# Kernel optimization log

Measured on AMD Instinct MI355X. Metric: run time of the kernel, lower is better.

Reference implementation:

```python
import jax, jax.numpy as jnp
import numpy as np

V, S, B, D, H, DH, FF = 98304, 1536, 2, 768, 24, 32, 3072
SCALE = 1.0 / float(np.sqrt(DH))  # 0.17677669529663687


def _ln(x, w, b, eps=1e-5):
    mu = jnp.mean(x, axis=-1, keepdims=True)
    var = jnp.mean(jnp.square(x - mu), axis=-1, keepdims=True)
    return (x - mu) * jax.lax.rsqrt(var + eps) * w + b


def _block(x, mask, ln1w, ln1b, wqkv, bqkv, wo, bo, ln2w, ln2b, wfc, bfc, wproj, bproj):
    # x: (S, B, D) Megatron layout; mask: (B, 1, S, S) bool, True = masked
    h = _ln(x, ln1w, ln1b)
    qkv = (h @ wqkv.T + bqkv).reshape(S, B, H, 3 * DH)  # interleaved q/k/v per head
    q, k, v = qkv[..., :DH], qkv[..., DH:2 * DH], qkv[..., 2 * DH:]
    q = jnp.transpose(q, (1, 2, 0, 3))  # (B, H, S, DH)
    k = jnp.transpose(k, (1, 2, 0, 3))
    v = jnp.transpose(v, (1, 2, 0, 3))
    scores = jnp.einsum('bhqd,bhkd->bhqk', q, k) * SCALE  # (B, H, S, S)
    scores = jnp.where(mask, jnp.float32(-10000.0), scores)
    p = jax.nn.softmax(scores, axis=-1)
    ctx = jnp.einsum('bhqk,bhkd->bhqd', p, v)
    ctx = jnp.transpose(ctx, (2, 0, 1, 3)).reshape(S, B, D)  # back to (S, B, D)
    x = x + ctx @ wo.T + bo  # attention residual (dropout treated as identity)
    h2 = _ln(x, ln2w, ln2b)
    m = jax.nn.gelu(h2 @ wfc.T + bfc, approximate=False)  # exact (erf) gelu as aten.gelu
    return x + m @ wproj.T + bproj


def _param_shapes():
    ps = [('wte', (V, D)), ('wpe', (S, D))]
    for l in ('l0', 'l1'):
        ps += [(l + '_ln1_w', (D,)), (l + '_ln1_b', (D,)),
               (l + '_wqkv', (3 * D, D)), (l + '_bqkv', (3 * D,)),
               (l + '_wo', (D, D)), (l + '_bo', (D,)),
               (l + '_ln2_w', (D,)), (l + '_ln2_b', (D,)),
               (l + '_wfc', (FF, D)), (l + '_bfc', (FF,)),
               (l + '_wproj', (D, FF)), (l + '_bproj', (D,))]
    ps += [('lnf_w', (D,)), ('lnf_b', (D,))]
    return ps


def setup_inputs() -> dict:
    key = jax.random.key(0)
    inp = {}
    inp['input_ids'] = jax.random.randint(jax.random.fold_in(key, 0), (B, S), 0, V, dtype=jnp.int32)
    inp['position_ids'] = jnp.broadcast_to(jnp.arange(S, dtype=jnp.int32), (B, S))
    causal = jnp.triu(jnp.ones((S, S), jnp.bool_), k=1)  # True above diagonal = masked
    inp['attn_mask'] = jnp.broadcast_to(causal, (B, 1, S, S))
    for i, (name, shape) in enumerate(_param_shapes()):
        k = jax.random.fold_in(key, 100 + i)
        if name in ('lnf_w',) or (('_ln' in name) and name.endswith('_w')):
            inp[name] = jnp.ones(shape, jnp.float32)
        else:
            inp[name] = jax.random.normal(k, shape, jnp.float32) * 0.02
    return inp


def reference(input_ids, position_ids, attn_mask,
              wte, wpe,
              l0_ln1_w, l0_ln1_b, l0_wqkv, l0_bqkv, l0_wo, l0_bo,
              l0_ln2_w, l0_ln2_b, l0_wfc, l0_bfc, l0_wproj, l0_bproj,
              l1_ln1_w, l1_ln1_b, l1_wqkv, l1_bqkv, l1_wo, l1_bo,
              l1_ln2_w, l1_ln2_b, l1_wfc, l1_bfc, l1_wproj, l1_bproj,
              lnf_w, lnf_b):
    x = wte[input_ids] + wpe[position_ids]  # (B, S, D)
    x = jnp.transpose(x, (1, 0, 2))  # (S, B, D)
    x = _block(x, attn_mask, l0_ln1_w, l0_ln1_b, l0_wqkv, l0_bqkv, l0_wo, l0_bo,
               l0_ln2_w, l0_ln2_b, l0_wfc, l0_bfc, l0_wproj, l0_bproj)
    x = _block(x, attn_mask, l1_ln1_w, l1_ln1_b, l1_wqkv, l1_bqkv, l1_wo, l1_bo,
               l1_ln2_w, l1_ln2_b, l1_wfc, l1_bfc, l1_wproj, l1_bproj)
    return _ln(x, lnf_w, lnf_b)  # (S, B, D)
```

## Files before the change

### kernel.cpp

```cpp
#include <hip/hip_runtime.h>
#include <cmath>
#include <type_traits>

typedef unsigned short u16;
typedef float  f32x4 __attribute__((ext_vector_type(4)));
typedef short  s16x8 __attribute__((ext_vector_type(8)));
typedef __bf16 b16x8 __attribute__((ext_vector_type(8)));

#define GLOBAL_AS __attribute__((address_space(1)))
#define LDS_AS    __attribute__((address_space(3)))

constexpr int S_  = 1536;
constexpr int B_  = 2;
constexpr int D_  = 768;
constexpr int H_  = 24;
constexpr int DH_ = 32;
constexpr int FF_ = 3072;
constexpr int N_  = S_ * B_;
constexpr int D3_ = 3 * D_;
constexpr float SCALE_ = 0.17677669529663687f;

template <typename T>
static __device__ inline auto mfma_try(T a, T b, f32x4 c, int)
    -> decltype(__builtin_amdgcn_mfma_f32_16x16x32_bf16(a, b, c, 0, 0, 0)) {
  return __builtin_amdgcn_mfma_f32_16x16x32_bf16(a, b, c, 0, 0, 0);
}
template <typename T>
static __device__ inline f32x4 mfma_try(T a, T b, f32x4 c, long) {
  b16x8 ab = __builtin_bit_cast(b16x8, a);
  b16x8 bb = __builtin_bit_cast(b16x8, b);
  return __builtin_amdgcn_mfma_f32_16x16x32_bf16(ab, bb, c, 0, 0, 0);
}
static __device__ inline f32x4 mfma_bf16(s16x8 a, s16x8 b, f32x4 c) {
  return mfma_try(a, b, c, 0);
}

static __device__ inline u16 f2bf(float f) {
  unsigned u = __builtin_bit_cast(unsigned, f);
  return (u16)((u + 0x7FFFu + ((u >> 16) & 1u)) >> 16);
}

static __device__ inline float rmax16(float v) {
  v = fmaxf(v, __shfl_xor(v, 1));
  v = fmaxf(v, __shfl_xor(v, 2));
  v = fmaxf(v, __shfl_xor(v, 4));
  v = fmaxf(v, __shfl_xor(v, 8));
  return v;
}
static __device__ inline float rsum16(float v) {
  v += __shfl_xor(v, 1);
  v += __shfl_xor(v, 2);
  v += __shfl_xor(v, 4);
  v += __shfl_xor(v, 8);
  return v;
}

__global__ void convert_weights_kernel(const float* __restrict__ wqkv,
                                       const float* __restrict__ wo,
                                       const float* __restrict__ wfc,
                                       const float* __restrict__ wproj,
                                       u16* __restrict__ dst) {
  constexpr int C0 = D3_ * D_;
  constexpr int C1 = C0 + D_ * D_;
  constexpr int C2 = C1 + FF_ * D_;
  constexpr int C3 = C2 + D_ * FF_;
  int i4 = (blockIdx.x * 256 + threadIdx.x) * 4;
  if (i4 >= C3) return;
  const float* src; int off;
  if (i4 < C0)      { src = wqkv;  off = i4; }
  else if (i4 < C1) { src = wo;    off = i4 - C0; }
  else if (i4 < C2) { src = wfc;   off = i4 - C1; }
  else              { src = wproj; off = i4 - C2; }
  float4 v = *(const float4*)(src + off);
  ushort4 o;
  o.x = f2bf(v.x); o.y = f2bf(v.y); o.z = f2bf(v.z); o.w = f2bf(v.w);
  *(ushort4*)(dst + i4) = o;
}

__global__ void embed_kernel(const int* __restrict__ ids, const int* __restrict__ pos,
                             const float* __restrict__ wte, const float* __restrict__ wpe,
                             float* __restrict__ x) {
  int g  = blockIdx.x * 256 + threadIdx.x;
  int i4 = g * 4;
  int row = i4 / D_;
  int d   = i4 - row * D_;
  int s = row >> 1, b = row & 1;
  int t = ids[b * S_ + s];
  int p = pos[b * S_ + s];
  float4 a = *(const float4*)(wte + (size_t)t * D_ + d);
  float4 c = *(const float4*)(wpe + (size_t)p * D_ + d);
  a.x += c.x; a.y += c.y; a.z += c.z; a.w += c.w;
  *(float4*)(x + i4) = a;
}

template <typename OUT>
__global__ void ln_kernel(const float* __restrict__ x, const float* __restrict__ w,
                          const float* __restrict__ b, OUT* __restrict__ out) {
  int wid = threadIdx.x >> 6, lane = threadIdx.x & 63;
  int tok = blockIdx.x * 4 + wid;
  const float* xr = x + (size_t)tok * D_;
  float4 v[3];
  float s = 0.f, ss = 0.f;
#pragma unroll
  for (int c = 0; c < 3; ++c) {
    v[c] = *(const float4*)(xr + c * 256 + lane * 4);
    s  += v[c].x + v[c].y + v[c].z + v[c].w;
    ss += v[c].x * v[c].x + v[c].y * v[c].y + v[c].z * v[c].z + v[c].w * v[c].w;
  }
#pragma unroll
  for (int m = 1; m <= 32; m <<= 1) { s += __shfl_xor(s, m); ss += __shfl_xor(ss, m); }
  float mu = s * (1.0f / D_);
  float var = ss * (1.0f / D_) - mu * mu;
  float rs = rsqrtf(var + 1e-5f);
#pragma unroll
  for (int c = 0; c < 3; ++c) {
    int d = c * 256 + lane * 4;
    float o0 = (v[c].x - mu) * rs * w[d + 0] + b[d + 0];
    float o1 = (v[c].y - mu) * rs * w[d + 1] + b[d + 1];
    float o2 = (v[c].z - mu) * rs * w[d + 2] + b[d + 2];
    float o3 = (v[c].w - mu) * rs * w[d + 3] + b[d + 3];
    if constexpr (std::is_same_v<OUT, u16>) {
      ushort4 o; o.x = f2bf(o0); o.y = f2bf(o1); o.z = f2bf(o2); o.w = f2bf(o3);
      *(ushort4*)(out + (size_t)tok * D_ + d) = o;
    } else {
      float4 o; o.x = o0; o.y = o1; o.z = o2; o.w = o3;
      *(float4*)(out + (size_t)tok * D_ + d) = o;
    }
  }
}

template <int BM, int BN, int EPI>
__launch_bounds__(256, 3)
__global__ void gemm_kernel(const u16* __restrict__ X, const u16* __restrict__ W,
                            const float* __restrict__ bias, int K,
                            u16* __restrict__ o0, u16* __restrict__ o1,
                            u16* __restrict__ o2, float* __restrict__ xio) {
  constexpr int BK = 64;
  constexpr int WM = BM / 2, WN = BN / 2, TM = WM / 16, TN = WN / 16;
  __shared__ u16 As[BM * BK];
  __shared__ u16 Bs[BN * BK];
  const int tid = threadIdx.x;
  const int wid = tid >> 6, lane = tid & 63;
  const int col = lane & 15, quad = lane >> 4;
  const int wm = wid & 1, wn = wid >> 1;
  const int rowA0 = blockIdx.x * BM;
  const int rowB0 = blockIdx.y * BN;

  f32x4 zz = {0.f, 0.f, 0.f, 0.f};
  f32x4 acc[TM][TN];
#pragma unroll
  for (int i = 0; i < TM; ++i)
#pragma unroll
    for (int j = 0; j < TN; ++j) acc[i][j] = zz;

  for (int k0 = 0; k0 < K; k0 += BK) {
#pragma unroll
    for (int it = 0; it < BM / 32; ++it) {
      int bs = (it * 4 + wid) * 64;
      int slot = bs + lane;
      int r = slot >> 3;
      int c = (slot & 7) ^ (r & 7);
      const u16* g = &X[(size_t)(rowA0 + r) * K + k0 + c * 8];
      __builtin_amdgcn_global_load_lds((const GLOBAL_AS unsigned int*)g,
                                       (LDS_AS unsigned int*)&As[bs * 8], 16, 0, 0);
    }
#pragma unroll
    for (int it = 0; it < BN / 32; ++it) {
      int bs = (it * 4 + wid) * 64;
      int slot = bs + lane;
      int r = slot >> 3;
      int c = (slot & 7) ^ (r & 7);
      const u16* g = &W[(size_t)(rowB0 + r) * K + k0 + c * 8];
      __builtin_amdgcn_global_load_lds((const GLOBAL_AS unsigned int*)g,
                                       (LDS_AS unsigned int*)&Bs[bs * 8], 16, 0, 0);
    }
    __syncthreads();
#pragma unroll
    for (int kb = 0; kb < 2; ++kb) {
      s16x8 af[TM], bf[TN];
#pragma unroll
      for (int ti = 0; ti < TM; ++ti) {
        int row = wm * WM + ti * 16 + col;
        af[ti] = *(const s16x8*)&As[row * BK + ((kb * 4 + quad) ^ (row & 7)) * 8];
      }
#pragma unroll
      for (int tj = 0; tj < TN; ++tj) {
        int row = wn * WN + tj * 16 + col;
        bf[tj] = *(const s16x8*)&Bs[row * BK + ((kb * 4 + quad) ^ (row & 7)) * 8];
      }
#pragma unroll
      for (int ti = 0; ti < TM; ++ti)
#pragma unroll
        for (int tj = 0; tj < TN; ++tj)
          acc[ti][tj] = mfma_bf16(af[ti], bf[tj], acc[ti][tj]);
    }
    __syncthreads();
  }

  const int tokBase  = rowA0 + wm * WM + quad * 4;
  const int featBase = rowB0 + wn * WN + col;
#pragma unroll
  for (int ti = 0; ti < TM; ++ti) {
#pragma unroll
    for (int tj = 0; tj < TN; ++tj) {
      int feat = featBase + tj * 16;
      float bv = bias[feat];
#pragma unroll
      for (int r = 0; r < 4; ++r) {
        int tok = tokBase + ti * 16 + r;
        float v = acc[ti][tj][r] + bv;
        if constexpr (EPI == 0) {
          int hh = feat / 96;
          int rem = feat - hh * 96;
          int comp = rem >> 5, d = rem & 31;
          int s = tok >> 1, bb = tok & 1;
          int bh = bb * H_ + hh;
          if (comp == 0)      o0[((size_t)bh * S_ + s) * DH_ + d] = f2bf(v);
          else if (comp == 1) o1[((size_t)bh * S_ + s) * DH_ + d] = f2bf(v);
          else                o2[((size_t)bh * DH_ + d) * S_ + s] = f2bf(v);
        } else if constexpr (EPI == 1) {
          float* p = xio + (size_t)tok * D_ + feat;
          *p = *p + v;
        } else {
          float g = 0.5f * v * (1.0f + erff(v * 0.70710678118654752f));
          o0[(size_t)tok * FF_ + feat] = f2bf(g);
        }
      }
    }
  }
}

__launch_bounds__(256)
__global__ void attn_kernel(const u16* __restrict__ q, const u16* __restrict__ k,
                            const u16* __restrict__ vt, u16* __restrict__ ctx) {
  __shared__ u16 Plds[4][16 * 40];
  const int tid = threadIdx.x;
  const int wid = tid >> 6, lane = tid & 63;
  const int col = lane & 15, quad = lane >> 4;
  const int bh = blockIdx.y;
  const int bb = bh / H_, hh = bh - bb * H_;
  const u16* qb = q  + (size_t)bh * S_ * DH_;
  const u16* kb = k  + (size_t)bh * S_ * DH_;
  const u16* vb = vt + (size_t)bh * DH_ * S_;
  const int q0 = blockIdx.x * 64 + wid * 16;

  s16x8 qf = *(const s16x8*)&qb[(q0 + col) * DH_ + quad * 8];
  f32x4 zz = {0.f, 0.f, 0.f, 0.f};
  f32x4 o0 = zz, o1 = zz;
  float mr[4] = {-1e30f, -1e30f, -1e30f, -1e30f};
  float lr[4] = {0.f, 0.f, 0.f, 0.f};

  const int kend = q0 + 16;
  for (int k0 = 0; k0 < kend; k0 += 32) {
    s16x8 kf0 = *(const s16x8*)&kb[(k0 + col) * DH_ + quad * 8];
    s16x8 kf1 = *(const s16x8*)&kb[(k0 + 16 + col) * DH_ + quad * 8];
    f32x4 s0 = mfma_bf16(qf, kf0, zz);
    f32x4 s1 = mfma_bf16(qf, kf1, zz);
#pragma unroll
    for (int r = 0; r < 4; ++r) {
      int qq = q0 + quad * 4 + r;
      float x0 = (k0 + col <= qq)      ? s0[r] * SCALE_ : -10000.0f;
      float x1 = (k0 + 16 + col <= qq) ? s1[r] * SCALE_ : -10000.0f;
      float cm = rmax16(fmaxf(x0, x1));
      float nm = fmaxf(mr[r], cm);
      float al = __expf(mr[r] - nm);
      float p0 = __expf(x0 - nm);
      float p1 = __expf(x1 - nm);
      float rs = rsum16(p0 + p1);
      lr[r] = lr[r] * al + rs;
      mr[r] = nm;
      o0[r] *= al; o1[r] *= al;
      Plds[wid][(quad * 4 + r) * 40 + col]      = f2bf(p0);
      Plds[wid][(quad * 4 + r) * 40 + 16 + col] = f2bf(p1);
    }
    __builtin_amdgcn_wave_barrier();
    __builtin_amdgcn_s_waitcnt(0xc07f);
    __builtin_amdgcn_wave_barrier();
    s16x8 pf  = *(const s16x8*)&Plds[wid][col * 40 + quad * 8];
    s16x8 vf0 = *(const s16x8*)&vb[(size_t)col * S_ + k0 + quad * 8];
    s16x8 vf1 = *(const s16x8*)&vb[(size_t)(16 + col) * S_ + k0 + quad * 8];
    o0 = mfma_bf16(pf, vf0, o0);
    o1 = mfma_bf16(pf, vf1, o1);
    __builtin_amdgcn_wave_barrier();
  }
#pragma unroll
  for (int r = 0; r < 4; ++r) {
    float inv = 1.0f / lr[r];
    int qq = q0 + quad * 4 + r;
    size_t base = ((size_t)qq * B_ + bb) * D_ + hh * DH_;
    ctx[base + col]      = f2bf(o0[r] * inv);
    ctx[base + 16 + col] = f2bf(o1[r] * inv);
  }
}

extern "C" void kernel_launch(void* const* d_in, const int* in_sizes, int n_in,
                              void* d_out, int out_size, void* d_ws, size_t ws_size,
                              hipStream_t stream) {
  const int*   ids = (const int*)d_in[0];
  const int*   pos = (const int*)d_in[1];
  const float* wte = (const float*)d_in[3];
  const float* wpe = (const float*)d_in[4];
  const float* lnf_w = (const float*)d_in[29];
  const float* lnf_b = (const float*)d_in[30];

  char* ws = (char*)d_ws;
  constexpr size_t SZ_X   = (size_t)N_ * D_ * 4;
  constexpr size_t SZ_H   = (size_t)N_ * D_ * 2;
  constexpr size_t SZ_QKV = (size_t)B_ * H_ * S_ * DH_ * 2;
  constexpr size_t SZ_M   = (size_t)N_ * FF_ * 2;
  constexpr int    WELEM  = D3_ * D_ + D_ * D_ + FF_ * D_ + D_ * FF_;

  float* xbuf = (float*)ws;
  u16* hbuf  = (u16*)(ws + SZ_X);
  u16* qbuf  = (u16*)(ws + SZ_X + SZ_H);
  u16* kbuf  = (u16*)(ws + SZ_X + SZ_H + SZ_QKV);
  u16* vtbuf = (u16*)(ws + SZ_X + SZ_H + 2 * SZ_QKV);
  u16* cbuf  = (u16*)(ws + SZ_X + SZ_H + 3 * SZ_QKV);
  u16* mbuf  = (u16*)(ws + SZ_X + SZ_H + 4 * SZ_QKV);
  u16* wbf   = (u16*)(ws + SZ_X + SZ_H + 4 * SZ_QKV + SZ_M);

  embed_kernel<<<N_ * D_ / 4 / 256, 256, 0, stream>>>(ids, pos, wte, wpe, xbuf);

  for (int l = 0; l < 2; ++l) {
    int p = 5 + l * 12;
    const float* ln1w  = (const float*)d_in[p + 0];
    const float* ln1b  = (const float*)d_in[p + 1];
    const float* wqkv  = (const float*)d_in[p + 2];
    const float* bqkv  = (const float*)d_in[p + 3];
    const float* wo    = (const float*)d_in[p + 4];
    const float* bo    = (const float*)d_in[p + 5];
    const float* ln2w  = (const float*)d_in[p + 6];
    const float* ln2b  = (const float*)d_in[p + 7];
    const float* wfc   = (const float*)d_in[p + 8];
    const float* bfc   = (const float*)d_in[p + 9];
    const float* wproj = (const float*)d_in[p + 10];
    const float* bproj = (const float*)d_in[p + 11];

    u16* wb = wbf + (size_t)l * WELEM;
    u16* wqkv_b  = wb;
    u16* wo_b    = wb + D3_ * D_;
    u16* wfc_b   = wb + D3_ * D_ + D_ * D_;
    u16* wproj_b = wb + D3_ * D_ + D_ * D_ + FF_ * D_;

    convert_weights_kernel<<<WELEM / 4 / 256, 256, 0, stream>>>(wqkv, wo, wfc, wproj, wb);

    ln_kernel<u16><<<N_ / 4, 256, 0, stream>>>(xbuf, ln1w, ln1b, hbuf);
    gemm_kernel<128, 128, 0><<<dim3(N_ / 128, D3_ / 128), 256, 0, stream>>>(
        hbuf, wqkv_b, bqkv, D_, qbuf, kbuf, vtbuf, nullptr);
    attn_kernel<<<dim3(S_ / 64, B_ * H_), 256, 0, stream>>>(qbuf, kbuf, vtbuf, cbuf);
    gemm_kernel<128, 64, 1><<<dim3(N_ / 128, D_ / 64), 256, 0, stream>>>(
        cbuf, wo_b, bo, D_, nullptr, nullptr, nullptr, xbuf);
    ln_kernel<u16><<<N_ / 4, 256, 0, stream>>>(xbuf, ln2w, ln2b, hbuf);
    gemm_kernel<128, 128, 2><<<dim3(N_ / 128, FF_ / 128), 256, 0, stream>>>(
        hbuf, wfc_b, bfc, D_, mbuf, nullptr, nullptr, nullptr);
    gemm_kernel<128, 64, 1><<<dim3(N_ / 128, D_ / 64), 256, 0, stream>>>(
        mbuf, wproj_b, bproj, FF_, nullptr, nullptr, nullptr, xbuf);
  }

  ln_kernel<float><<<N_ / 4, 256, 0, stream>>>(xbuf, lnf_w, lnf_b, (float*)d_out);
}
```

Before: 843.6 us.

## Fuse embed with first LN, batch weight conversion, and widen attention key tiles

Merges the embedding add with the first layer norm and converts both layers' weights in a single launch instead of two, which removes kernel launches and one pass over the activations. The attention scale is folded into Q in the QKV epilogue. Attention now handles fully unmasked key blocks in 64-wide tiles without mask checks, leaving the narrower masked loop only for the diagonal region. LN weights are loaded as float4 and f2bf uses the builtin bf16 conversion. Folding the scale before rounding to bf16 slightly changes numerics.

```diff
diff --git a/kernel.cpp b/kernel.cpp
--- a/kernel.cpp
+++ b/kernel.cpp
@@ -36,8 +36,7 @@
 }
 
 static __device__ inline u16 f2bf(float f) {
-  unsigned u = __builtin_bit_cast(unsigned, f);
-  return (u16)((u + 0x7FFFu + ((u >> 16) & 1u)) >> 16);
+  return __builtin_bit_cast(u16, (__bf16)f);
 }
 
 static __device__ inline float rmax16(float v) {
@@ -55,17 +54,22 @@
   return v;
 }
 
-__global__ void convert_weights_kernel(const float* __restrict__ wqkv,
-                                       const float* __restrict__ wo,
-                                       const float* __restrict__ wfc,
-                                       const float* __restrict__ wproj,
+__global__ void convert_weights_kernel(const float* __restrict__ q0, const float* __restrict__ o0,
+                                       const float* __restrict__ f0, const float* __restrict__ p0,
+                                       const float* __restrict__ q1, const float* __restrict__ o1,
+                                       const float* __restrict__ f1, const float* __restrict__ p1,
                                        u16* __restrict__ dst) {
   constexpr int C0 = D3_ * D_;
   constexpr int C1 = C0 + D_ * D_;
   constexpr int C2 = C1 + FF_ * D_;
   constexpr int C3 = C2 + D_ * FF_;
+  const int l = blockIdx.y;
   int i4 = (blockIdx.x * 256 + threadIdx.x) * 4;
   if (i4 >= C3) return;
+  const float* wqkv  = l ? q1 : q0;
+  const float* wo    = l ? o1 : o0;
+  const float* wfc   = l ? f1 : f0;
+  const float* wproj = l ? p1 : p0;
   const float* src; int off;
   if (i4 < C0)      { src = wqkv;  off = i4; }
   else if (i4 < C1) { src = wo;    off = i4 - C0; }
@@ -74,23 +78,51 @@
   float4 v = *(const float4*)(src + off);
   ushort4 o;
   o.x = f2bf(v.x); o.y = f2bf(v.y); o.z = f2bf(v.z); o.w = f2bf(v.w);
-  *(ushort4*)(dst + i4) = o;
-}
-
-__global__ void embed_kernel(const int* __restrict__ ids, const int* __restrict__ pos,
-                             const float* __restrict__ wte, const float* __restrict__ wpe,
-                             float* __restrict__ x) {
-  int g  = blockIdx.x * 256 + threadIdx.x;
-  int i4 = g * 4;
-  int row = i4 / D_;
-  int d   = i4 - row * D_;
-  int s = row >> 1, b = row & 1;
-  int t = ids[b * S_ + s];
-  int p = pos[b * S_ + s];
-  float4 a = *(const float4*)(wte + (size_t)t * D_ + d);
-  float4 c = *(const float4*)(wpe + (size_t)p * D_ + d);
-  a.x += c.x; a.y += c.y; a.z += c.z; a.w += c.w;
-  *(float4*)(x + i4) = a;
+  *(ushort4*)(dst + (size_t)l * C3 + i4) = o;
+}
+
+__global__ void embed_ln_kernel(const int* __restrict__ ids, const int* __restrict__ pos,
+                                const float* __restrict__ wte, const float* __restrict__ wpe,
+                                const float* __restrict__ w, const float* __restrict__ b,
+                                float* __restrict__ x, u16* __restrict__ h) {
+  int wid = threadIdx.x >> 6, lane = threadIdx.x & 63;
+  int tok = blockIdx.x * 4 + wid;
+  int s = tok >> 1, bb = tok & 1;
+  int t = ids[bb * S_ + s];
+  int p = pos[bb * S_ + s];
+  const float* wt = wte + (size_t)t * D_;
+  const float* wp = wpe + (size_t)p * D_;
+  float* xr = x + (size_t)tok * D_;
+  float4 v[3];
+  float sum = 0.f, ss = 0.f;
+#pragma unroll
+  for (int c = 0; c < 3; ++c) {
+    int d = c * 256 + lane * 4;
+    float4 a = *(const float4*)(wt + d);
+    float4 e = *(const float4*)(wp + d);
+    a.x += e.x; a.y += e.y; a.z += e.z; a.w += e.w;
+    v[c] = a;
+    *(float4*)(xr + d) = a;
+    sum += a.x + a.y + a.z + a.w;
+    ss  += a.x * a.x + a.y * a.y + a.z * a.z + a.w * a.w;
+  }
+#pragma unroll
+  for (int m = 1; m <= 32; m <<= 1) { sum += __shfl_xor(sum, m); ss += __shfl_xor(ss, m); }
+  float mu = sum * (1.0f / D_);
+  float var = ss * (1.0f / D_) - mu * mu;
+  float rs = rsqrtf(var + 1e-5f);
+#pragma unroll
+  for (int c = 0; c < 3; ++c) {
+    int d = c * 256 + lane * 4;
+    float4 wv = *(const float4*)(w + d);
+    float4 bv = *(const float4*)(b + d);
+    ushort4 o;
+    o.x = f2bf((v[c].x - mu) * rs * wv.x + bv.x);
+    o.y = f2bf((v[c].y - mu) * rs * wv.y + bv.y);
+    o.z = f2bf((v[c].z - mu) * rs * wv.z + bv.z);
+    o.w = f2bf((v[c].w - mu) * rs * wv.w + bv.w);
+    *(ushort4*)(h + (size_t)tok * D_ + d) = o;
+  }
 }
 
 template <typename OUT>
@@ -115,10 +147,12 @@
 #pragma unroll
   for (int c = 0; c < 3; ++c) {
     int d = c * 256 + lane * 4;
-    float o0 = (v[c].x - mu) * rs * w[d + 0] + b[d + 0];
-    float o1 = (v[c].y - mu) * rs * w[d + 1] + b[d + 1];
-    float o2 = (v[c].z - mu) * rs * w[d + 2] + b[d + 2];
-    float o3 = (v[c].w - mu) * rs * w[d + 3] + b[d + 3];
+    float4 wv = *(const float4*)(w + d);
+    float4 bv = *(const float4*)(b + d);
+    float o0 = (v[c].x - mu) * rs * wv.x + bv.x;
+    float o1 = (v[c].y - mu) * rs * wv.y + bv.y;
+    float o2 = (v[c].z - mu) * rs * wv.z + bv.z;
+    float o3 = (v[c].w - mu) * rs * wv.w + bv.w;
     if constexpr (std::is_same_v<OUT, u16>) {
       ushort4 o; o.x = f2bf(o0); o.y = f2bf(o1); o.z = f2bf(o2); o.w = f2bf(o3);
       *(ushort4*)(out + (size_t)tok * D_ + d) = o;
@@ -215,7 +249,7 @@
           int comp = rem >> 5, d = rem & 31;
           int s = tok >> 1, bb = tok & 1;
           int bh = bb * H_ + hh;
-          if (comp == 0)      o0[((size_t)bh * S_ + s) * DH_ + d] = f2bf(v);
+          if (comp == 0)      o0[((size_t)bh * S_ + s) * DH_ + d] = f2bf(v * SCALE_);
           else if (comp == 1) o1[((size_t)bh * S_ + s) * DH_ + d] = f2bf(v);
           else                o2[((size_t)bh * DH_ + d) * S_ + s] = f2bf(v);
         } else if constexpr (EPI == 1) {
@@ -233,7 +267,7 @@
 __launch_bounds__(256)
 __global__ void attn_kernel(const u16* __restrict__ q, const u16* __restrict__ k,
                             const u16* __restrict__ vt, u16* __restrict__ ctx) {
-  __shared__ u16 Plds[4][16 * 40];
+  __shared__ u16 Plds[4][16 * 72];
   const int tid = threadIdx.x;
   const int wid = tid >> 6, lane = tid & 63;
   const int col = lane & 15, quad = lane >> 4;
@@ -243,6 +277,7 @@
   const u16* kb = k  + (size_t)bh * S_ * DH_;
   const u16* vb = vt + (size_t)bh * DH_ * S_;
   const int q0 = blockIdx.x * 64 + wid * 16;
+  u16* P = &Plds[wid][0];
 
   s16x8 qf = *(const s16x8*)&qb[(q0 + col) * DH_ + quad * 8];
   f32x4 zz = {0.f, 0.f, 0.f, 0.f};
@@ -250,8 +285,54 @@
   float mr[4] = {-1e30f, -1e30f, -1e30f, -1e30f};
   float lr[4] = {0.f, 0.f, 0.f, 0.f};
 
+  const int fullEnd = (q0 >> 6) << 6;
+  for (int k0 = 0; k0 < fullEnd; k0 += 64) {
+    s16x8 kf0 = *(const s16x8*)&kb[(k0 +  0 + col) * DH_ + quad * 8];
+    s16x8 kf1 = *(const s16x8*)&kb[(k0 + 16 + col) * DH_ + quad * 8];
+    s16x8 kf2 = *(const s16x8*)&kb[(k0 + 32 + col) * DH_ + quad * 8];
+    s16x8 kf3 = *(const s16x8*)&kb[(k0 + 48 + col) * DH_ + quad * 8];
+    f32x4 s0 = mfma_bf16(qf, kf0, zz);
+    f32x4 s1 = mfma_bf16(qf, kf1, zz);
+    f32x4 s2 = mfma_bf16(qf, kf2, zz);
+    f32x4 s3 = mfma_bf16(qf, kf3, zz);
+#pragma unroll
+    for (int r = 0; r < 4; ++r) {
+      float a0 = s0[r], a1 = s1[r], a2 = s2[r], a3 = s3[r];
+      float cm = rmax16(fmaxf(fmaxf(a0, a1), fmaxf(a2, a3)));
+      float nm = fmaxf(mr[r], cm);
+      float al = __expf(mr[r] - nm);
+      float p0 = __expf(a0 - nm);
+      float p1 = __expf(a1 - nm);
+      float p2 = __expf(a2 - nm);
+      float p3 = __expf(a3 - nm);
+      float rs = rsum16((p0 + p1) + (p2 + p3));
+      lr[r] = lr[r] * al + rs;
+      mr[r] = nm;
+      o0[r] *= al; o1[r] *= al;
+      int ro = (quad * 4 + r) * 72;
+      P[ro + col]      = f2bf(p0);
+      P[ro + col + 16] = f2bf(p1);
+      P[ro + col + 32] = f2bf(p2);
+      P[ro + col + 48] = f2bf(p3);
+    }
+    __builtin_amdgcn_wave_barrier();
+    __builtin_amdgcn_s_waitcnt(0xc07f);
+    __builtin_amdgcn_wave_barrier();
+    s16x8 pf0 = *(const s16x8*)&P[col * 72 + quad * 8];
+    s16x8 pf1 = *(const s16x8*)&P[col * 72 + 32 + quad * 8];
+    s16x8 va0 = *(const s16x8*)&vb[(size_t)col * S_ + k0 + quad * 8];
+    s16x8 va1 = *(const s16x8*)&vb[(size_t)col * S_ + k0 + 32 + quad * 8];
+    s16x8 vc0 = *(const s16x8*)&vb[(size_t)(16 + col) * S_ + k0 + quad * 8];
+    s16x8 vc1 = *(const s16x8*)&vb[(size_t)(16 + col) * S_ + k0 + 32 + quad * 8];
+    o0 = mfma_bf16(pf0, va0, o0);
+    o0 = mfma_bf16(pf1, va1, o0);
+    o1 = mfma_bf16(pf0, vc0, o1);
+    o1 = mfma_bf16(pf1, vc1, o1);
+    __builtin_amdgcn_wave_barrier();
+  }
+
   const int kend = q0 + 16;
-  for (int k0 = 0; k0 < kend; k0 += 32) {
+  for (int k0 = fullEnd; k0 < kend; k0 += 32) {
     s16x8 kf0 = *(const s16x8*)&kb[(k0 + col) * DH_ + quad * 8];
     s16x8 kf1 = *(const s16x8*)&kb[(k0 + 16 + col) * DH_ + quad * 8];
     f32x4 s0 = mfma_bf16(qf, kf0, zz);
@@ -259,8 +340,8 @@
 #pragma unroll
     for (int r = 0; r < 4; ++r) {
       int qq = q0 + quad * 4 + r;
-      float x0 = (k0 + col <= qq)      ? s0[r] * SCALE_ : -10000.0f;
-      float x1 = (k0 + 16 + col <= qq) ? s1[r] * SCALE_ : -10000.0f;
+      float x0 = (k0 + col <= qq)      ? s0[r] : -10000.0f;
+      float x1 = (k0 + 16 + col <= qq) ? s1[r] : -10000.0f;
       float cm = rmax16(fmaxf(x0, x1));
       float nm = fmaxf(mr[r], cm);
       float al = __expf(mr[r] - nm);
@@ -270,19 +351,21 @@
       lr[r] = lr[r] * al + rs;
       mr[r] = nm;
       o0[r] *= al; o1[r] *= al;
-      Plds[wid][(quad * 4 + r) * 40 + col]      = f2bf(p0);
-      Plds[wid][(quad * 4 + r) * 40 + 16 + col] = f2bf(p1);
+      int ro = (quad * 4 + r) * 72;
+      P[ro + col]      = f2bf(p0);
+      P[ro + col + 16] = f2bf(p1);
     }
     __builtin_amdgcn_wave_barrier();
     __builtin_amdgcn_s_waitcnt(0xc07f);
     __builtin_amdgcn_wave_barrier();
-    s16x8 pf  = *(const s16x8*)&Plds[wid][col * 40 + quad * 8];
+    s16x8 pf  = *(const s16x8*)&P[col * 72 + quad * 8];
     s16x8 vf0 = *(const s16x8*)&vb[(size_t)col * S_ + k0 + quad * 8];
     s16x8 vf1 = *(const s16x8*)&vb[(size_t)(16 + col) * S_ + k0 + quad * 8];
     o0 = mfma_bf16(pf, vf0, o0);
     o1 = mfma_bf16(pf, vf1, o1);
     __builtin_amdgcn_wave_barrier();
   }
+
 #pragma unroll
   for (int r = 0; r < 4; ++r) {
     float inv = 1.0f / lr[r];
@@ -319,21 +402,24 @@
   u16* mbuf  = (u16*)(ws + SZ_X + SZ_H + 4 * SZ_QKV);
   u16* wbf   = (u16*)(ws + SZ_X + SZ_H + 4 * SZ_QKV + SZ_M);
 
-  embed_kernel<<<N_ * D_ / 4 / 256, 256, 0, stream>>>(ids, pos, wte, wpe, xbuf);
+  convert_weights_kernel<<<dim3(WELEM / 4 / 256, 2), 256, 0, stream>>>(
+      (const float*)d_in[7],  (const float*)d_in[9],
+      (const float*)d_in[13], (const float*)d_in[15],
+      (const float*)d_in[19], (const float*)d_in[21],
+      (const float*)d_in[25], (const float*)d_in[27], wbf);
+
+  embed_ln_kernel<<<N_ / 4, 256, 0, stream>>>(
+      ids, pos, wte, wpe, (const float*)d_in[5], (const float*)d_in[6], xbuf, hbuf);
 
   for (int l = 0; l < 2; ++l) {
     int p = 5 + l * 12;
     const float* ln1w  = (const float*)d_in[p + 0];
     const float* ln1b  = (const float*)d_in[p + 1];
-    const float* wqkv  = (const float*)d_in[p + 2];
     const float* bqkv  = (const float*)d_in[p + 3];
-    const float* wo    = (const float*)d_in[p + 4];
     const float* bo    = (const float*)d_in[p + 5];
     const float* ln2w  = (const float*)d_in[p + 6];
     const float* ln2b  = (const float*)d_in[p + 7];
-    const float* wfc   = (const float*)d_in[p + 8];
     const float* bfc   = (const float*)d_in[p + 9];
-    const float* wproj = (const float*)d_in[p + 10];
     const float* bproj = (const float*)d_in[p + 11];
 
     u16* wb = wbf + (size_t)l * WELEM;
@@ -342,9 +428,9 @@
     u16* wfc_b   = wb + D3_ * D_ + D_ * D_;
     u16* wproj_b = wb + D3_ * D_ + D_ * D_ + FF_ * D_;
 
-    convert_weights_kernel<<<WELEM / 4 / 256, 256, 0, stream>>>(wqkv, wo, wfc, wproj, wb);
-
-    ln_kernel<u16><<<N_ / 4, 256, 0, stream>>>(xbuf, ln1w, ln1b, hbuf);
+    if (l > 0) {
+      ln_kernel<u16><<<N_ / 4, 256, 0, stream>>>(xbuf, ln1w, ln1b, hbuf);
+    }
     gemm_kernel<128, 128, 0><<<dim3(N_ / 128, D3_ / 128), 256, 0, stream>>>(
         hbuf, wqkv_b, bqkv, D_, qbuf, kbuf, vtbuf, nullptr);
     attn_kernel<<<dim3(S_ / 64, B_ * H_), 256, 0, stream>>>(qbuf, kbuf, vtbuf, cbuf);
```

Result: faster. 805.5 us (-4.5%).
